# Optimization experiments

Hardware: AMD Instinct MI355X
Metric: run time of the kernel (lower is better)

## Reference

```python
import jax, jax.numpy as jnp
import numpy as np

B, CIN, C, H, T = 8, 64, 64, 62, 400
S = 32              # StateSpaceLayer state_dim default
MID = max(1, C // 16)  # ChannelAttention reduction=16


def _dwconv(x, w, pad):
    # x [B,C,H,W], w [C,1,kh,kw], depthwise conv
    return jax.lax.conv_general_dilated(
        x, w, (1, 1), pad,
        dimension_numbers=('NCHW', 'OIHW', 'NCHW'),
        feature_group_count=x.shape[1])


def _pw(x, w):  # 1x1 conv, w [O,C]
    return jnp.einsum('bchw,oc->bohw', x, w)


def _bn(x, g, b):  # eval-mode BatchNorm with running mean=0, var=1 folded into affine
    return x * g[None, :, None, None] + b[None, :, None, None]


def _chan_attn(x, w1, w2):
    # AdaptiveAvg/MaxPool(1) -> shared MLP -> sigmoid gate
    avg = x.mean(axis=(2, 3))
    mx = x.max(axis=(2, 3))
    fc = lambda v: jax.nn.relu(v @ w1.T) @ w2.T  # Linear weights are [out,in]
    a = jax.nn.sigmoid(fc(avg) + fc(mx))
    return x * a[:, :, None, None]


def _spat_attn(x, w):
    avg = x.mean(axis=1, keepdims=True)
    mx = x.max(axis=1, keepdims=True)
    comb = jnp.concatenate([avg, mx], axis=1)  # [B,2,H,W]
    a = jax.nn.sigmoid(jax.lax.conv_general_dilated(
        comb, w, (1, 1), ((3, 3), (3, 3)),
        dimension_numbers=('NCHW', 'OIHW', 'NCHW')))
    return x * a


def _ssm(x, A, Bv, Cm, D, ln_g, ln_b):
    # Faithful to torch: raw reshape [B,C,H,T] -> [B*H, C, T] (row-major, same as torch)
    b, c, h, t = x.shape
    xs = x.reshape(b * h, c, t)
    seq = jnp.moveaxis(xs, 2, 0)  # [T, N, C]

    def step(state, inp):
        state = state @ A.T + Bv               # state = state A^T + B
        out = jax.nn.gelu(state @ Cm + inp * D, approximate=False)
        return state, out

    init = jnp.zeros((b * h, A.shape[0]), x.dtype)
    _, outs = jax.lax.scan(step, init, seq)    # outs [T, N, C]
    out = jnp.moveaxis(outs, 0, 2).reshape(b, c, h, t)
    out = x + out  # residual (dropout p=0)
    # LayerNorm over channel dim
    y = jnp.moveaxis(out, 1, -1)  # [B,H,T,C]
    mu = y.mean(-1, keepdims=True)
    var = ((y - mu) ** 2).mean(-1, keepdims=True)
    y = (y - mu) / jnp.sqrt(var + 1e-5) * ln_g + ln_b
    return jnp.moveaxis(y, -1, 1)


def _half(x, dwdw, dwpw, dwg, dwb, caw1, caw2, saw,
          d1dw, d1pw, d1g, d1b, A, Bv, Cm, D, lng, lnb):
    pad5 = ((2, 2), (2, 2))
    b1 = jax.nn.relu(_bn(_pw(_dwconv(x, dwdw[0], pad5), dwpw[0]), dwg[0], dwb[0]))
    b2 = jax.nn.relu(_bn(_pw(_dwconv(x, dwdw[1], pad5), dwpw[1]), dwg[1], dwb[1]))
    cb = b1 * _chan_attn(b1, caw1, caw2)       # note: x * ChannelAttention(x) as in source
    cb = _bn(_pw(_dwconv(cb, d1dw, ((0, 0), (1, 1))), d1pw), d1g, d1b)
    cb = jax.nn.sigmoid(cb)
    sb = jax.nn.sigmoid(b2 * _spat_attn(b2, saw))
    return _ssm(cb, A, Bv, Cm, D, lng, lnb) * sb


def setup_inputs() -> dict:
    key = jax.random.key(0)
    ks = jax.random.split(key, 16)
    n = lambda k, shp, s=0.1: jax.random.normal(k, shp, dtype=jnp.float32) * s
    return {
        'x': jax.random.normal(ks[0], (B, CIN, H, T), dtype=jnp.float32),
        'in_w': n(ks[1], (C, CIN)),
        'dw2d_dw': n(ks[2], (2, 2, C, 1, 5, 5)),
        'dw2d_pw': n(ks[3], (2, 2, C, C)),
        'dw2d_g': jnp.ones((2, 2, C), jnp.float32),
        'dw2d_b': jnp.zeros((2, 2, C), jnp.float32),
        'ca_w1': n(ks[4], (2, MID, C)),
        'ca_w2': n(ks[5], (2, C, MID)),
        'sa_w': n(ks[6], (2, 1, 2, 7, 7)),
        'dw1d_dw': n(ks[7], (2, C, 1, 1, 3)),
        'dw1d_pw': n(ks[8], (2, C, C)),
        'dw1d_g': jnp.ones((2, C), jnp.float32),
        'dw1d_b': jnp.zeros((2, C), jnp.float32),
        'ssm_A': n(ks[9], (2, S, S)),
        'ssm_B': n(ks[10], (2, S)),
        'ssm_C': n(ks[11], (2, S, C)),
        'ssm_D': n(ks[12], (2, C)),
        'ln_g': jnp.ones((2, C), jnp.float32),
        'ln_b': jnp.zeros((2, C), jnp.float32),
        'out_w': n(ks[13], (C, C)),
        'out_g': jnp.ones((C,), jnp.float32),
        'out_b': jnp.zeros((C,), jnp.float32),
    }


def reference(x, in_w, dw2d_dw, dw2d_pw, dw2d_g, dw2d_b, ca_w1, ca_w2, sa_w,
              dw1d_dw, dw1d_pw, dw1d_g, dw1d_b, ssm_A, ssm_B, ssm_C, ssm_D,
              ln_g, ln_b, out_w, out_g, out_b):
    h = _pw(x, in_w)
    o = _half(h, dw2d_dw[0], dw2d_pw[0], dw2d_g[0], dw2d_b[0], ca_w1[0], ca_w2[0],
              sa_w[0], dw1d_dw[0], dw1d_pw[0], dw1d_g[0], dw1d_b[0],
              ssm_A[0], ssm_B[0], ssm_C[0], ssm_D[0], ln_g[0], ln_b[0])
    o = o[..., ::-1]  # flip time axis
    o = _half(o, dw2d_dw[1], dw2d_pw[1], dw2d_g[1], dw2d_b[1], ca_w1[1], ca_w2[1],
              sa_w[1], dw1d_dw[1], dw1d_pw[1], dw1d_g[1], dw1d_b[1],
              ssm_A[1], ssm_B[1], ssm_C[1], ssm_D[1], ln_g[1], ln_b[1])
    o = o[..., ::-1]
    return jax.nn.relu(_bn(_pw(o, out_w), out_g, out_b))
```

## Files before the change

kernel.cpp:

```cpp
#include <hip/hip_runtime.h>
#include <math.h>

#define DI __device__ __forceinline__

constexpr int B_ = 8, C_ = 64, H_ = 62, T_ = 400, S_ = 32;
constexpr int HT   = H_ * T_;
constexpr int CHT  = C_ * HT;
constexpr int NPOS = B_ * HT;
constexpr int NTOT = B_ * CHT;

typedef __attribute__((ext_vector_type(8))) short short8;
typedef __attribute__((ext_vector_type(4))) float float4v;

DI float sigmoidf_(float x) { return 1.f / (1.f + expf(-x)); }
DI float gelu_(float x) { return 0.5f * x * (1.f + erff(x * 0.70710678118654752f)); }

template<int ACT> DI float act_(float v) {
  if (ACT == 1) return fmaxf(v, 0.f);
  if (ACT == 2) return sigmoidf_(v);
  return v;
}

DI unsigned short f2b(float f) {
  unsigned int u = __float_as_uint(f);
  u += 0x7FFFu + ((u >> 16) & 1u);
  return (unsigned short)(u >> 16);
}
DI unsigned int pk2(float a, float b) {
  return (unsigned int)f2b(a) | ((unsigned int)f2b(b) << 16);
}

__global__ __launch_bounds__(256) void prep(const float* __restrict__ in_w,
    const float* __restrict__ dwpw, const float* __restrict__ dwg,
    const float* __restrict__ d1pw, const float* __restrict__ d1g,
    const float* __restrict__ outw, const float* __restrict__ outg,
    unsigned short* __restrict__ wf) {
  int idx = blockIdx.x * 256 + threadIdx.x;
  int lane = idx & 63, kc = (idx >> 6) & 1, w = (idx >> 7) & 3, slot = idx >> 9;
  const float* src; const float* g;
  switch (slot) {
    case 0: src = in_w;            g = nullptr;      break;
    case 1: src = dwpw + 0 * 4096; g = dwg + 0 * 64; break;
    case 2: src = dwpw + 1 * 4096; g = dwg + 1 * 64; break;
    case 3: src = d1pw + 0 * 4096; g = d1g + 0 * 64; break;
    case 4: src = dwpw + 2 * 4096; g = dwg + 2 * 64; break;
    case 5: src = dwpw + 3 * 4096; g = dwg + 3 * 64; break;
    case 6: src = d1pw + 1 * 4096; g = d1g + 1 * 64; break;
    default: src = outw;           g = outg;         break;
  }
  int o = w * 16 + (lane & 15);
  float gv = g ? g[o] : 1.f;
  unsigned int pack[4];
  #pragma unroll
  for (int h = 0; h < 4; ++h) {
    int c = kc * 32 + (lane >> 4) * 8 + h * 2;
    pack[h] = pk2(src[o * 64 + c] * gv, src[o * 64 + c + 1] * gv);
  }
  *(uint4*)&wf[idx * 8] = make_uint4(pack[0], pack[1], pack[2], pack[3]);
}

template<int ACT, bool REV, bool SPAT, bool DW13>
__global__ __launch_bounds__(256) void pwk(const float* __restrict__ in,
    const unsigned short* __restrict__ wf, const float* __restrict__ bb,
    const float* __restrict__ ac, const float* __restrict__ w3,
    float* __restrict__ out, float* __restrict__ comb) {
  __shared__ unsigned short Xb[64 * 72];
  const int tid = threadIdx.x;
  const int lane = tid & 63;
  const int wv = tid >> 6;
  const int p0 = blockIdx.x * 64;
  {
    const int ps = (tid & 15) * 4;
    const int cs = (tid >> 4) * 4;
    const int p4 = p0 + ps;
    const int b = p4 / HT, ht = p4 - b * HT;
    const int row = ht / T_, t0 = ht - row * T_;
    const float* rp0 = in + b * CHT + row * T_;
    float xv[4][4];
    #pragma unroll
    for (int cj = 0; cj < 4; ++cj) {
      const int c = cs + cj;
      const float* rp = rp0 + c * HT;
      if constexpr (DW13) {
        float4 xc = *(const float4*)&rp[t0];
        float xm = (t0 > 0)       ? rp[t0 - 1] : 0.f;
        float xp = (t0 < T_ - 4)  ? rp[t0 + 4] : 0.f;
        float s0 = xm * xm, s1 = xc.x * xc.x, s2 = xc.y * xc.y;
        float s3 = xc.z * xc.z, s4 = xc.w * xc.w, s5 = xp * xp;
        float acv = ac[b * 64 + c];
        float c0 = w3[c * 3 + 0] * acv, c1 = w3[c * 3 + 1] * acv,
              c2 = w3[c * 3 + 2] * acv;
        xv[cj][0] = c0 * s0 + c1 * s1 + c2 * s2;
        xv[cj][1] = c0 * s1 + c1 * s2 + c2 * s3;
        xv[cj][2] = c0 * s2 + c1 * s3 + c2 * s4;
        xv[cj][3] = c0 * s3 + c1 * s4 + c2 * s5;
      } else if constexpr (REV) {
        float4 u = *(const float4*)&rp[T_ - 4 - t0];
        xv[cj][0] = u.w; xv[cj][1] = u.z; xv[cj][2] = u.y; xv[cj][3] = u.x;
      } else {
        float4 u = *(const float4*)&rp[t0];
        xv[cj][0] = u.x; xv[cj][1] = u.y; xv[cj][2] = u.z; xv[cj][3] = u.w;
      }
    }
    #pragma unroll
    for (int pi = 0; pi < 4; ++pi) {
      int r = ps + pi;
      int col = cs ^ (((r >> 2) & 7) << 3);
      *(uint2*)&Xb[r * 72 + col] =
          make_uint2(pk2(xv[0][pi], xv[1][pi]), pk2(xv[2][pi], xv[3][pi]));
    }
  }
  short8 af0 = *(const short8*)(wf + ((wv * 2 + 0) * 64 + lane) * 8);
  short8 af1 = *(const short8*)(wf + ((wv * 2 + 1) * 64 + lane) * 8);
  const int m4 = (lane >> 4) * 4;
  float binit[4];
  #pragma unroll
  for (int j = 0; j < 4; ++j) binit[j] = bb ? bb[wv * 16 + m4 + j] : 0.f;
  __syncthreads();
  float4v acc[4];
  #pragma unroll
  for (int nt = 0; nt < 4; ++nt) { acc[nt][0] = acc[nt][1] = acc[nt][2] = acc[nt][3] = 0.f; }
  #pragma unroll
  for (int nt = 0; nt < 4; ++nt) {
    int r = nt * 16 + (lane & 15);
    int sw = ((r >> 2) & 7) << 3;
    int cb0 = ((lane >> 4) * 8) ^ sw;
    int cb1 = (32 + (lane >> 4) * 8) ^ sw;
    short8 b0 = *(const short8*)&Xb[r * 72 + cb0];
    short8 b1 = *(const short8*)&Xb[r * 72 + cb1];
    acc[nt] = __builtin_amdgcn_mfma_f32_16x16x32_bf16(af0, b0, acc[nt], 0, 0, 0);
    acc[nt] = __builtin_amdgcn_mfma_f32_16x16x32_bf16(af1, b1, acc[nt], 0, 0, 0);
  }
  float psum[4], pmaxv[4];
  #pragma unroll
  for (int nt = 0; nt < 4; ++nt) {
    int n = nt * 16 + (lane & 15);
    int p = p0 + n;
    int b = p / HT, ht = p - b * HT;
    float* op = out + b * CHT + ht + (wv * 16 + m4) * HT;
    float s = 0.f, m = -3.4e38f;
    #pragma unroll
    for (int j = 0; j < 4; ++j) {
      float r = act_<ACT>(acc[nt][j] + binit[j]);
      op[j * HT] = r;
      if constexpr (SPAT) { s += r; m = fmaxf(m, r); }
    }
    if constexpr (SPAT) {
      s += __shfl_xor(s, 16); s += __shfl_xor(s, 32);
      m = fmaxf(m, __shfl_xor(m, 16)); m = fmaxf(m, __shfl_xor(m, 32));
      psum[nt] = s; pmaxv[nt] = m;
    }
  }
  if constexpr (SPAT) {
    __shared__ float redS[4][64], redM[4][64];
    if (lane < 16) {
      #pragma unroll
      for (int nt = 0; nt < 4; ++nt) {
        redS[wv][nt * 16 + lane] = psum[nt];
        redM[wv][nt * 16 + lane] = pmaxv[nt];
      }
    }
    __syncthreads();
    if (tid < 64) {
      float s = redS[0][tid] + redS[1][tid] + redS[2][tid] + redS[3][tid];
      float m = fmaxf(fmaxf(redM[0][tid], redM[1][tid]),
                      fmaxf(redM[2][tid], redM[3][tid]));
      int pp = p0 + tid;
      int b2 = pp / HT, ht2 = pp - b2 * HT;
      comb[b2 * 2 * HT + ht2] = s * (1.f / 64.f);
      comb[b2 * 2 * HT + HT + ht2] = m;
    }
  }
}

__global__ __launch_bounds__(256) void dw5dual(const float* __restrict__ in,
    const float* __restrict__ w0_, const float* __restrict__ w1_,
    float* __restrict__ out0, float* __restrict__ out1) {
  const int bc = blockIdx.y;
  const int c = bc & 63;
  int task = blockIdx.x * 256 + threadIdx.x;
  if (task >= 6200) return;
  int h = task / 100;
  int t0 = (task - h * 100) << 2;
  const float* base = in + bc * HT;
  float win[5][12];
  const bool fast = (t0 >= 4) && (t0 <= 392);
  #pragma unroll
  for (int u = 0; u < 5; ++u) {
    int hh = h + u - 2;
    if (hh >= 0 && hh < H_) {
      const float* row = base + hh * T_;
      if (fast) {
        #pragma unroll
        for (int j = 0; j < 3; ++j)
          *(float4*)&win[u][4 * j] = *(const float4*)&row[t0 - 4 + 4 * j];
      } else {
        #pragma unroll
        for (int k = 0; k < 12; ++k) {
          int tt = t0 - 4 + k;
          win[u][k] = (tt >= 0 && tt < T_) ? row[tt] : 0.f;
        }
      }
    } else {
      #pragma unroll
      for (int k = 0; k < 12; ++k) win[u][k] = 0.f;
    }
  }
  float o0[4] = {0.f, 0.f, 0.f, 0.f};
  float o1[4] = {0.f, 0.f, 0.f, 0.f};
  #pragma unroll
  for (int u = 0; u < 5; ++u)
    #pragma unroll
    for (int v = 0; v < 5; ++v) {
      float wa = w0_[c * 25 + u * 5 + v];
      float wb = w1_[c * 25 + u * 5 + v];
      #pragma unroll
      for (int j = 0; j < 4; ++j) {
        float x = win[u][j + v + 2];
        o0[j] += wa * x;
        o1[j] += wb * x;
      }
    }
  *(float4*)&out0[bc * HT + h * T_ + t0] = make_float4(o0[0], o0[1], o0[2], o0[3]);
  *(float4*)&out1[bc * HT + h * T_ + t0] = make_float4(o1[0], o1[1], o1[2], o1[3]);
}

__global__ __launch_bounds__(256) void chanred(const float* __restrict__ in,
    float* __restrict__ sum_, float* __restrict__ max_) {
  int bc = blockIdx.x >> 1, hf = blockIdx.x & 1;
  const float* base = in + (size_t)bc * HT + hf * (HT / 2);
  float s = 0.f, m = -3.4e38f;
  for (int i = threadIdx.x; i < HT / 2; i += 256) {
    float v = base[i];
    s += v; m = fmaxf(m, v);
  }
  #pragma unroll
  for (int off = 32; off > 0; off >>= 1) {
    s += __shfl_down(s, off);
    m = fmaxf(m, __shfl_down(m, off));
  }
  __shared__ float ss[4], sm[4];
  int wv = threadIdx.x >> 6;
  if ((threadIdx.x & 63) == 0) { ss[wv] = s; sm[wv] = m; }
  __syncthreads();
  if (threadIdx.x == 0) {
    float S = ss[0] + ss[1] + ss[2] + ss[3];
    float M = fmaxf(fmaxf(sm[0], sm[1]), fmaxf(sm[2], sm[3]));
    sum_[hf * 512 + bc] = S;
    max_[hf * 512 + bc] = M;
  }
}

__global__ __launch_bounds__(512) void cafc(const float* __restrict__ cs,
    const float* __restrict__ cm, const float* __restrict__ w1,
    const float* __restrict__ w2, float* __restrict__ ac) {
  __shared__ float sa[512], sx[512], hsum[8][4];
  int tid = threadIdx.x;
  sa[tid] = (cs[tid] + cs[512 + tid]) * (1.f / HT);
  sx[tid] = fmaxf(cm[tid], cm[512 + tid]);
  __syncthreads();
  if (tid < 32) {
    int b = tid >> 2, m = tid & 3;
    float s1 = 0.f, s2 = 0.f;
    #pragma unroll
    for (int cc = 0; cc < 64; ++cc) {
      float wv = w1[m * 64 + cc];
      s1 += sa[b * 64 + cc] * wv;
      s2 += sx[b * 64 + cc] * wv;
    }
    hsum[b][m] = fmaxf(s1, 0.f) + fmaxf(s2, 0.f);
  }
  __syncthreads();
  int b = tid >> 6, cc = tid & 63;
  float f = 0.f;
  #pragma unroll
  for (int m = 0; m < 4; ++m) f += hsum[b][m] * w2[cc * 4 + m];
  ac[tid] = sigmoidf_(f);
}

__global__ __launch_bounds__(256) void conv7(const float* __restrict__ comb,
    const float* __restrict__ w, float* __restrict__ as_) {
  __shared__ float sm[2][8][408];
  __shared__ float sw[98];
  const int b = blockIdx.x / 31, hp = blockIdx.x % 31;
  const int h0 = hp * 2;
  const float* cb0 = comb + b * 2 * HT;
  const int tid = threadIdx.x;
  if (tid < 98) sw[tid] = w[tid];
  for (int e = tid; e < 2 * 8 * 408; e += 256) {
    int ci = e / 3264, rem = e - ci * 3264;
    int r = rem / 408, tt = rem - r * 408;
    int hh = h0 - 3 + r, t = tt - 4;
    float v = 0.f;
    if (hh >= 0 && hh < H_ && t >= 0 && t < T_) v = cb0[ci * HT + hh * T_ + t];
    sm[ci][r][tt] = v;
  }
  __syncthreads();
  for (int o = tid; o < 800; o += 256) {
    int oh = o / 400, ot = o - oh * 400;
    float acc = 0.f;
    #pragma unroll
    for (int ci = 0; ci < 2; ++ci)
      #pragma unroll
      for (int u = 0; u < 7; ++u)
        #pragma unroll
        for (int v = 0; v < 7; ++v)
          acc += sw[ci * 49 + u * 7 + v] * sm[ci][oh + u][ot + v + 1];
    as_[b * HT + (h0 + oh) * T_ + ot] = sigmoidf_(acc);
  }
}

__global__ __launch_bounds__(1024) void ssmctA(const float* __restrict__ A_,
    const float* __restrict__ Bv_, float* __restrict__ Pg, float* __restrict__ qg) {
  const int hf = blockIdx.x;
  const float* A = A_ + hf * 1024;
  const float* Bv = Bv_ + hf * 32;
  __shared__ float Pbuf[2][32 * 33];
  __shared__ float qbuf[2][32];
  const int tid = threadIdx.x;
  float* Pc = Pbuf[0]; float* Pn = Pbuf[1];
  float* qc = qbuf[0]; float* qn = qbuf[1];
  Pc[(tid >> 5) * 33 + (tid & 31)] = A[tid];
  if (tid < 32) qc[tid] = Bv[tid];
  __syncthreads();
  for (int i = 0; i < 9; ++i) {
    Pg[(hf * 9 + i) * 1024 + tid] = Pc[(tid >> 5) * 33 + (tid & 31)];
    if (tid < 32) qg[(hf * 9 + i) * 32 + tid] = qc[tid];
    if (i == 8) break;
    const int r = tid >> 5, cc = tid & 31;
    float s0 = 0.f, s1 = 0.f, s2 = 0.f, s3 = 0.f;
    #pragma unroll
    for (int k = 0; k < 32; k += 4) {
      s0 += Pc[r * 33 + k + 0] * Pc[(k + 0) * 33 + cc];
      s1 += Pc[r * 33 + k + 1] * Pc[(k + 1) * 33 + cc];
      s2 += Pc[r * 33 + k + 2] * Pc[(k + 2) * 33 + cc];
      s3 += Pc[r * 33 + k + 3] * Pc[(k + 3) * 33 + cc];
    }
    float qv = 0.f;
    if (tid < 32) {
      float a0 = 0.f, a1 = 0.f;
      #pragma unroll
      for (int k = 0; k < 32; k += 2) {
        a0 += Pc[tid * 33 + k] * qc[k];
        a1 += Pc[tid * 33 + k + 1] * qc[k + 1];
      }
      qv = qc[tid] + a0 + a1;
    }
    Pn[r * 33 + cc] = s0 + s1 + s2 + s3;
    if (tid < 32) qn[tid] = qv;
    __syncthreads();
    float* tp = Pc; Pc = Pn; Pn = tp;
    float* tq = qc; qc = qn; qn = tq;
  }
}

__global__ __launch_bounds__(1024) void ssmctB(const float* __restrict__ Pg,
    const float* __restrict__ qg, const float* __restrict__ Cm_,
    float* __restrict__ ct) {
  const int hf = blockIdx.y;
  __shared__ float P[9][32][33];
  __shared__ float q[9][32];
  __shared__ float Cs[32 * 64];
  __shared__ float st[32][33];
  const int tid = threadIdx.x;
  #pragma unroll
  for (int i = 0; i < 9; ++i) {
    int rem = tid;
    P[i][rem >> 5][rem & 31] = Pg[(hf * 9 + i) * 1024 + rem];
  }
  if (tid < 9 * 32) q[tid >> 5][tid & 31] = qg[hf * 9 * 32 + tid];
  for (int e = tid; e < 2048; e += 1024) Cs[e] = Cm_[hf * 2048 + e];
  __syncthreads();
  const int grp = tid >> 5, j = tid & 31;
  const int tIdx = blockIdx.x * 32 + grp;
  const int n = tIdx + 1;
  float s = 0.f;
  #pragma unroll
  for (int i = 0; i < 9; ++i) {
    st[grp][j] = s;
    float a0 = q[i][j], a1 = 0.f;
    #pragma unroll
    for (int k = 0; k < 32; k += 2) {
      a0 += P[i][j][k] * st[grp][k];
      a1 += P[i][j][k + 1] * st[grp][k + 1];
    }
    s = ((n >> i) & 1) ? (a0 + a1) : s;
  }
  st[grp][j] = s;
  __syncthreads();
  #pragma unroll
  for (int e0 = 0; e0 < 2048; e0 += 1024) {
    int e = e0 + tid;
    int ts = e >> 6, c = e & 63;
    float a0 = 0.f, a1 = 0.f;
    #pragma unroll
    for (int k = 0; k < 32; k += 2) {
      a0 += st[ts][k] * Cs[k * 64 + c];
      a1 += st[ts][k + 1] * Cs[(k + 1) * 64 + c];
    }
    int tg = blockIdx.x * 32 + ts;
    if (tg < T_) ct[(hf * T_ + tg) * 64 + c] = a0 + a1;
  }
}

__global__ __launch_bounds__(256) void k8(const float* __restrict__ cb,
    const float* __restrict__ b2, const float* __restrict__ as_,
    const float* __restrict__ ct, const float* __restrict__ D,
    const float* __restrict__ lng, const float* __restrict__ lnb,
    float* __restrict__ out, int rev) {
  __shared__ float ct_s[64 * 65];
  __shared__ float red[4 * 2 * 66];
  const int tid = threadIdx.x;
  const int pl = tid & 63, wg = tid >> 6;
  const int p0 = blockIdx.x * 64;
  #pragma unroll
  for (int k = 0; k < 16; ++k) {
    int idx = k * 256 + tid;
    int r = idx >> 6, c2 = idx & 63;
    int t = (p0 + r) % T_;
    ct_s[r * 65 + c2] = ct[t * C_ + c2];
  }
  const int p = p0 + pl;
  const int b = p / HT, ht = p - b * HT;
  const int h = ht / T_, t = ht - h * T_;
  __syncthreads();
  const float* cbp = cb + b * CHT + ht;
  const float* b2p = b2 + b * CHT + ht;
  float o[16];
  float sum = 0.f;
  #pragma unroll
  for (int i = 0; i < 16; ++i) {
    int c = wg * 16 + i;
    float xv = cbp[c * HT];
    int c2 = (62 * c + h) & 63;
    float u = ct_s[pl * 65 + c2] + xv * D[c2];
    float v = xv + gelu_(u);
    o[i] = v; sum += v;
  }
  red[wg * 132 + pl] = sum;
  __syncthreads();
  float S = red[0 * 132 + pl] + red[1 * 132 + pl] + red[2 * 132 + pl] + red[3 * 132 + pl];
  float mu = S * (1.f / 64.f);
  float vp = 0.f;
  #pragma unroll
  for (int i = 0; i < 16; ++i) { float d = o[i] - mu; vp += d * d; }
  red[wg * 132 + 66 + pl] = vp;
  __syncthreads();
  float Q = red[0 * 132 + 66 + pl] + red[1 * 132 + 66 + pl] +
            red[2 * 132 + 66 + pl] + red[3 * 132 + 66 + pl];
  float rstd = rsqrtf(Q * (1.f / 64.f) + 1e-5f);
  float av = as_[p];
  int htw = rev ? (h * T_ + (T_ - 1 - t)) : ht;
  float* op = out + b * CHT + htw;
  #pragma unroll
  for (int i = 0; i < 16; ++i) {
    int c = wg * 16 + i;
    float y = (o[i] - mu) * rstd * lng[c] + lnb[c];
    float bv = b2p[c * HT];
    op[c * HT] = y * sigmoidf_(bv * bv * av);
  }
}

extern "C" void kernel_launch(void* const* d_in, const int* in_sizes, int n_in,
                              void* d_out, int out_size, void* d_ws, size_t ws_size,
                              hipStream_t stream) {
  const float* x    = (const float*)d_in[0];
  const float* in_w = (const float*)d_in[1];
  const float* dwdw = (const float*)d_in[2];
  const float* dwpw = (const float*)d_in[3];
  const float* dwg  = (const float*)d_in[4];
  const float* dwb  = (const float*)d_in[5];
  const float* caw1 = (const float*)d_in[6];
  const float* caw2 = (const float*)d_in[7];
  const float* saw  = (const float*)d_in[8];
  const float* d1dw = (const float*)d_in[9];
  const float* d1pw = (const float*)d_in[10];
  const float* d1g  = (const float*)d_in[11];
  const float* d1b  = (const float*)d_in[12];
  const float* ssmA = (const float*)d_in[13];
  const float* ssmBv= (const float*)d_in[14];
  const float* ssmC = (const float*)d_in[15];
  const float* ssmD = (const float*)d_in[16];
  const float* lng  = (const float*)d_in[17];
  const float* lnb  = (const float*)d_in[18];
  const float* outw = (const float*)d_in[19];
  const float* outg = (const float*)d_in[20];
  const float* outb = (const float*)d_in[21];

  size_t need = (size_t)(3 * (size_t)NTOT + 2 * NPOS + NPOS + 1024 + 1024 + 512
                         + 2 * T_ * C_ + 2 * 9 * 1024 + 2 * 9 * 32 + 16384) * 4;
  if (ws_size < need) return;

  float* W0 = (float*)d_ws;
  float* W1 = W0 + NTOT;
  float* W2 = W1 + NTOT;
  float* comb  = W2 + NTOT;
  float* as_   = comb + 2 * NPOS;
  float* casum = as_ + NPOS;
  float* camax = casum + 1024;
  float* ac    = camax + 1024;
  float* ct    = ac + 512;
  float* Pg    = ct + 2 * T_ * C_;
  float* qg    = Pg + 2 * 9 * 1024;
  unsigned short* Wbf = (unsigned short*)(qg + 2 * 9 * 32);

  prep<<<16, 256, 0, stream>>>(in_w, dwpw, dwg, d1pw, d1g, outw, outg, Wbf);
  ssmctA<<<2, 1024, 0, stream>>>(ssmA, ssmBv, Pg, qg);
  ssmctB<<<dim3(13, 2), 1024, 0, stream>>>(Pg, qg, ssmC, ct);
  pwk<0, false, false, false><<<3100, 256, 0, stream>>>(x, Wbf + 0 * 4096, nullptr,
                                                        nullptr, nullptr, W0, nullptr);

  auto run_half = [&](int hf, float* X, float* Fa, float* Fb) {
    const float* dw0 = dwdw + (hf * 2 + 0) * C_ * 25;
    const float* dw1 = dwdw + (hf * 2 + 1) * C_ * 25;
    const float* b0  = dwb + (hf * 2 + 0) * C_;
    const float* b1w = dwb + (hf * 2 + 1) * C_;
    dw5dual<<<dim3(25, 512), 256, 0, stream>>>(X, dw0, dw1, Fa, Fb);
    pwk<1, false, false, false><<<3100, 256, 0, stream>>>(Fa, Wbf + (1 + hf * 3) * 4096,
                                                          b0, nullptr, nullptr, X, nullptr);
    pwk<1, false, true, false><<<3100, 256, 0, stream>>>(Fb, Wbf + (2 + hf * 3) * 4096,
                                                         b1w, nullptr, nullptr, Fa, comb);
    chanred<<<1024, 256, 0, stream>>>(X, casum, camax);
    cafc<<<1, 512, 0, stream>>>(casum, camax, caw1 + hf * 4 * 64, caw2 + hf * 64 * 4, ac);
    conv7<<<248, 256, 0, stream>>>(comb, saw + hf * 98, as_);
    pwk<2, false, false, true><<<3100, 256, 0, stream>>>(X, Wbf + (3 + hf * 3) * 4096,
                                                         d1b + hf * C_, ac,
                                                         d1dw + hf * C_ * 3, Fb, nullptr);
    k8<<<3100, 256, 0, stream>>>(Fb, Fa, as_, ct + hf * T_ * C_,
                                 ssmD + hf * C_, lng + hf * C_, lnb + hf * C_,
                                 X, hf == 0 ? 1 : 0);
  };

  run_half(0, W0, W1, W2);
  run_half(1, W0, W1, W2);
  pwk<1, true, false, false><<<3100, 256, 0, stream>>>(W0, Wbf + 7 * 4096, outb,
                                                       nullptr, nullptr,
                                                       (float*)d_out, nullptr);
}
```

Before: 421.4 us.

## Store all intermediate activation buffers in bf16 instead of fp32

Switches the three large workspace buffers (W0/W1/W2) from fp32 to bf16 across every producer and consumer kernel: the pointwise MFMA kernels, the depthwise 5x5 conv, the channel reduction and the SSM/LayerNorm kernel. Since the pipeline is memory-bound over roughly 50M-element tensors, this halves the global read and write traffic of every stage. The cost is extra rounding of intermediates, which lowers accuracy and could push results past tolerance.

```diff
diff --git a/kernel.cpp b/kernel.cpp
--- a/kernel.cpp
+++ b/kernel.cpp
@@ -11,6 +11,7 @@
 
 typedef __attribute__((ext_vector_type(8))) short short8;
 typedef __attribute__((ext_vector_type(4))) float float4v;
+typedef unsigned short bh;
 
 DI float sigmoidf_(float x) { return 1.f / (1.f + expf(-x)); }
 DI float gelu_(float x) { return 0.5f * x * (1.f + erff(x * 0.70710678118654752f)); }
@@ -21,11 +22,12 @@
   return v;
 }
 
-DI unsigned short f2b(float f) {
+DI bh f2b(float f) {
   unsigned int u = __float_as_uint(f);
   u += 0x7FFFu + ((u >> 16) & 1u);
-  return (unsigned short)(u >> 16);
-}
+  return (bh)(u >> 16);
+}
+DI float b2f(bh u) { return __uint_as_float(((unsigned int)u) << 16); }
 DI unsigned int pk2(float a, float b) {
   return (unsigned int)f2b(a) | ((unsigned int)f2b(b) << 16);
 }
@@ -34,7 +36,7 @@
     const float* __restrict__ dwpw, const float* __restrict__ dwg,
     const float* __restrict__ d1pw, const float* __restrict__ d1g,
     const float* __restrict__ outw, const float* __restrict__ outg,
-    unsigned short* __restrict__ wf) {
+    bh* __restrict__ wf) {
   int idx = blockIdx.x * 256 + threadIdx.x;
   int lane = idx & 63, kc = (idx >> 6) & 1, w = (idx >> 7) & 3, slot = idx >> 9;
   const float* src; const float* g;
@@ -59,12 +61,12 @@
   *(uint4*)&wf[idx * 8] = make_uint4(pack[0], pack[1], pack[2], pack[3]);
 }
 
-template<int ACT, bool REV, bool SPAT, bool DW13>
-__global__ __launch_bounds__(256) void pwk(const float* __restrict__ in,
-    const unsigned short* __restrict__ wf, const float* __restrict__ bb,
+template<int ACT, bool REV, bool SPAT, bool DW13, bool INF32, bool OUTF32>
+__global__ __launch_bounds__(256) void pwk(const void* __restrict__ in_,
+    const bh* __restrict__ wf, const float* __restrict__ bb,
     const float* __restrict__ ac, const float* __restrict__ w3,
-    float* __restrict__ out, float* __restrict__ comb) {
-  __shared__ unsigned short Xb[64 * 72];
+    void* __restrict__ out_, float* __restrict__ comb) {
+  __shared__ bh Xb[64 * 72];
   const int tid = threadIdx.x;
   const int lane = tid & 63;
   const int wv = tid >> 6;
@@ -75,18 +77,39 @@
     const int p4 = p0 + ps;
     const int b = p4 / HT, ht = p4 - b * HT;
     const int row = ht / T_, t0 = ht - row * T_;
-    const float* rp0 = in + b * CHT + row * T_;
-    float xv[4][4];
-    #pragma unroll
-    for (int cj = 0; cj < 4; ++cj) {
-      const int c = cs + cj;
-      const float* rp = rp0 + c * HT;
-      if constexpr (DW13) {
-        float4 xc = *(const float4*)&rp[t0];
-        float xm = (t0 > 0)       ? rp[t0 - 1] : 0.f;
-        float xp = (t0 < T_ - 4)  ? rp[t0 + 4] : 0.f;
-        float s0 = xm * xm, s1 = xc.x * xc.x, s2 = xc.y * xc.y;
-        float s3 = xc.z * xc.z, s4 = xc.w * xc.w, s5 = xp * xp;
+    unsigned int packed[4][2];
+    if constexpr (INF32) {
+      const float* rp0 = (const float*)in_ + b * CHT + row * T_;
+      float xv[4][4];
+      #pragma unroll
+      for (int cj = 0; cj < 4; ++cj) {
+        const float* rp = rp0 + (cs + cj) * HT;
+        if constexpr (REV) {
+          float4 u = *(const float4*)&rp[T_ - 4 - t0];
+          xv[cj][0] = u.w; xv[cj][1] = u.z; xv[cj][2] = u.y; xv[cj][3] = u.x;
+        } else {
+          float4 u = *(const float4*)&rp[t0];
+          xv[cj][0] = u.x; xv[cj][1] = u.y; xv[cj][2] = u.z; xv[cj][3] = u.w;
+        }
+      }
+      #pragma unroll
+      for (int pi = 0; pi < 4; ++pi) {
+        packed[pi][0] = pk2(xv[0][pi], xv[1][pi]);
+        packed[pi][1] = pk2(xv[2][pi], xv[3][pi]);
+      }
+    } else if constexpr (DW13) {
+      const bh* rp0 = (const bh*)in_ + b * CHT + row * T_;
+      float xv[4][4];
+      #pragma unroll
+      for (int cj = 0; cj < 4; ++cj) {
+        const int c = cs + cj;
+        const bh* rp = rp0 + c * HT;
+        ushort4 u = *(const ushort4*)&rp[t0];
+        float x0 = b2f(u.x), x1 = b2f(u.y), x2 = b2f(u.z), x3 = b2f(u.w);
+        float xm = (t0 > 0)      ? b2f(rp[t0 - 1]) : 0.f;
+        float xp = (t0 < T_ - 4) ? b2f(rp[t0 + 4]) : 0.f;
+        float s0 = xm * xm, s1 = x0 * x0, s2 = x1 * x1;
+        float s3 = x2 * x2, s4 = x3 * x3, s5 = xp * xp;
         float acv = ac[b * 64 + c];
         float c0 = w3[c * 3 + 0] * acv, c1 = w3[c * 3 + 1] * acv,
               c2 = w3[c * 3 + 2] * acv;
@@ -94,20 +117,38 @@
         xv[cj][1] = c0 * s1 + c1 * s2 + c2 * s3;
         xv[cj][2] = c0 * s2 + c1 * s3 + c2 * s4;
         xv[cj][3] = c0 * s3 + c1 * s4 + c2 * s5;
-      } else if constexpr (REV) {
-        float4 u = *(const float4*)&rp[T_ - 4 - t0];
-        xv[cj][0] = u.w; xv[cj][1] = u.z; xv[cj][2] = u.y; xv[cj][3] = u.x;
-      } else {
-        float4 u = *(const float4*)&rp[t0];
-        xv[cj][0] = u.x; xv[cj][1] = u.y; xv[cj][2] = u.z; xv[cj][3] = u.w;
+      }
+      #pragma unroll
+      for (int pi = 0; pi < 4; ++pi) {
+        packed[pi][0] = pk2(xv[0][pi], xv[1][pi]);
+        packed[pi][1] = pk2(xv[2][pi], xv[3][pi]);
+      }
+    } else {
+      const bh* rp0 = (const bh*)in_ + b * CHT + row * T_;
+      bh us[4][4];
+      #pragma unroll
+      for (int cj = 0; cj < 4; ++cj) {
+        const bh* rp = rp0 + (cs + cj) * HT;
+        ushort4 u;
+        if constexpr (REV) {
+          u = *(const ushort4*)&rp[T_ - 4 - t0];
+          us[cj][0] = u.w; us[cj][1] = u.z; us[cj][2] = u.y; us[cj][3] = u.x;
+        } else {
+          u = *(const ushort4*)&rp[t0];
+          us[cj][0] = u.x; us[cj][1] = u.y; us[cj][2] = u.z; us[cj][3] = u.w;
+        }
+      }
+      #pragma unroll
+      for (int pi = 0; pi < 4; ++pi) {
+        packed[pi][0] = (unsigned int)us[0][pi] | ((unsigned int)us[1][pi] << 16);
+        packed[pi][1] = (unsigned int)us[2][pi] | ((unsigned int)us[3][pi] << 16);
       }
     }
     #pragma unroll
     for (int pi = 0; pi < 4; ++pi) {
       int r = ps + pi;
       int col = cs ^ (((r >> 2) & 7) << 3);
-      *(uint2*)&Xb[r * 72 + col] =
-          make_uint2(pk2(xv[0][pi], xv[1][pi]), pk2(xv[2][pi], xv[3][pi]));
+      *(uint2*)&Xb[r * 72 + col] = make_uint2(packed[pi][0], packed[pi][1]);
     }
   }
   short8 af0 = *(const short8*)(wf + ((wv * 2 + 0) * 64 + lane) * 8);
@@ -137,13 +178,23 @@
     int n = nt * 16 + (lane & 15);
     int p = p0 + n;
     int b = p / HT, ht = p - b * HT;
-    float* op = out + b * CHT + ht + (wv * 16 + m4) * HT;
     float s = 0.f, m = -3.4e38f;
-    #pragma unroll
-    for (int j = 0; j < 4; ++j) {
-      float r = act_<ACT>(acc[nt][j] + binit[j]);
-      op[j * HT] = r;
-      if constexpr (SPAT) { s += r; m = fmaxf(m, r); }
+    if constexpr (OUTF32) {
+      float* op = (float*)out_ + b * CHT + ht + (wv * 16 + m4) * HT;
+      #pragma unroll
+      for (int j = 0; j < 4; ++j) {
+        float r = act_<ACT>(acc[nt][j] + binit[j]);
+        op[j * HT] = r;
+        if constexpr (SPAT) { s += r; m = fmaxf(m, r); }
+      }
+    } else {
+      bh* op = (bh*)out_ + b * CHT + ht + (wv * 16 + m4) * HT;
+      #pragma unroll
+      for (int j = 0; j < 4; ++j) {
+        float r = act_<ACT>(acc[nt][j] + binit[j]);
+        op[j * HT] = f2b(r);
+        if constexpr (SPAT) { s += r; m = fmaxf(m, r); }
+      }
     }
     if constexpr (SPAT) {
       s += __shfl_xor(s, 16); s += __shfl_xor(s, 32);
@@ -173,32 +224,35 @@
   }
 }
 
-__global__ __launch_bounds__(256) void dw5dual(const float* __restrict__ in,
+__global__ __launch_bounds__(256) void dw5dual(const bh* __restrict__ in,
     const float* __restrict__ w0_, const float* __restrict__ w1_,
-    float* __restrict__ out0, float* __restrict__ out1) {
+    bh* __restrict__ out0, bh* __restrict__ out1) {
   const int bc = blockIdx.y;
   const int c = bc & 63;
   int task = blockIdx.x * 256 + threadIdx.x;
   if (task >= 6200) return;
   int h = task / 100;
   int t0 = (task - h * 100) << 2;
-  const float* base = in + bc * HT;
+  const bh* base = in + bc * HT;
   float win[5][12];
   const bool fast = (t0 >= 4) && (t0 <= 392);
   #pragma unroll
   for (int u = 0; u < 5; ++u) {
     int hh = h + u - 2;
     if (hh >= 0 && hh < H_) {
-      const float* row = base + hh * T_;
+      const bh* row = base + hh * T_;
       if (fast) {
         #pragma unroll
-        for (int j = 0; j < 3; ++j)
-          *(float4*)&win[u][4 * j] = *(const float4*)&row[t0 - 4 + 4 * j];
+        for (int j = 0; j < 3; ++j) {
+          ushort4 q = *(const ushort4*)&row[t0 - 4 + 4 * j];
+          win[u][4 * j + 0] = b2f(q.x); win[u][4 * j + 1] = b2f(q.y);
+          win[u][4 * j + 2] = b2f(q.z); win[u][4 * j + 3] = b2f(q.w);
+        }
       } else {
         #pragma unroll
         for (int k = 0; k < 12; ++k) {
           int tt = t0 - 4 + k;
-          win[u][k] = (tt >= 0 && tt < T_) ? row[tt] : 0.f;
+          win[u][k] = (tt >= 0 && tt < T_) ? b2f(row[tt]) : 0.f;
         }
       }
     } else {
@@ -221,18 +275,22 @@
         o1[j] += wb * x;
       }
     }
-  *(float4*)&out0[bc * HT + h * T_ + t0] = make_float4(o0[0], o0[1], o0[2], o0[3]);
-  *(float4*)&out1[bc * HT + h * T_ + t0] = make_float4(o1[0], o1[1], o1[2], o1[3]);
-}
-
-__global__ __launch_bounds__(256) void chanred(const float* __restrict__ in,
+  ushort4 r0, r1;
+  r0.x = f2b(o0[0]); r0.y = f2b(o0[1]); r0.z = f2b(o0[2]); r0.w = f2b(o0[3]);
+  r1.x = f2b(o1[0]); r1.y = f2b(o1[1]); r1.z = f2b(o1[2]); r1.w = f2b(o1[3]);
+  *(ushort4*)&out0[bc * HT + h * T_ + t0] = r0;
+  *(ushort4*)&out1[bc * HT + h * T_ + t0] = r1;
+}
+
+__global__ __launch_bounds__(256) void chanred(const bh* __restrict__ in,
     float* __restrict__ sum_, float* __restrict__ max_) {
   int bc = blockIdx.x >> 1, hf = blockIdx.x & 1;
-  const float* base = in + (size_t)bc * HT + hf * (HT / 2);
+  const bh* base = in + (size_t)bc * HT + hf * (HT / 2);
   float s = 0.f, m = -3.4e38f;
-  for (int i = threadIdx.x; i < HT / 2; i += 256) {
-    float v = base[i];
-    s += v; m = fmaxf(m, v);
+  for (int i = threadIdx.x * 2; i < HT / 2; i += 512) {
+    ushort2 q = *(const ushort2*)&base[i];
+    float v0 = b2f(q.x), v1 = b2f(q.y);
+    s += v0 + v1; m = fmaxf(m, fmaxf(v0, v1));
   }
   #pragma unroll
   for (int off = 32; off > 0; off >>= 1) {
@@ -403,11 +461,11 @@
   }
 }
 
-__global__ __launch_bounds__(256) void k8(const float* __restrict__ cb,
-    const float* __restrict__ b2, const float* __restrict__ as_,
+__global__ __launch_bounds__(256) void k8(const bh* __restrict__ cb,
+    const bh* __restrict__ b2, const float* __restrict__ as_,
     const float* __restrict__ ct, const float* __restrict__ D,
     const float* __restrict__ lng, const float* __restrict__ lnb,
-    float* __restrict__ out, int rev) {
+    bh* __restrict__ out, int rev) {
   __shared__ float ct_s[64 * 65];
   __shared__ float red[4 * 2 * 66];
   const int tid = threadIdx.x;
@@ -424,14 +482,14 @@
   const int b = p / HT, ht = p - b * HT;
   const int h = ht / T_, t = ht - h * T_;
   __syncthreads();
-  const float* cbp = cb + b * CHT + ht;
-  const float* b2p = b2 + b * CHT + ht;
+  const bh* cbp = cb + b * CHT + ht;
+  const bh* b2p = b2 + b * CHT + ht;
   float o[16];
   float sum = 0.f;
   #pragma unroll
   for (int i = 0; i < 16; ++i) {
     int c = wg * 16 + i;
-    float xv = cbp[c * HT];
+    float xv = b2f(cbp[c * HT]);
     int c2 = (62 * c + h) & 63;
     float u = ct_s[pl * 65 + c2] + xv * D[c2];
     float v = xv + gelu_(u);
@@ -451,13 +509,13 @@
   float rstd = rsqrtf(Q * (1.f / 64.f) + 1e-5f);
   float av = as_[p];
   int htw = rev ? (h * T_ + (T_ - 1 - t)) : ht;
-  float* op = out + b * CHT + htw;
+  bh* op = out + b * CHT + htw;
   #pragma unroll
   for (int i = 0; i < 16; ++i) {
     int c = wg * 16 + i;
     float y = (o[i] - mu) * rstd * lng[c] + lnb[c];
-    float bv = b2p[c * HT];
-    op[c * HT] = y * sigmoidf_(bv * bv * av);
+    float bv = b2f(b2p[c * HT]);
+    op[c * HT] = f2b(y * sigmoidf_(bv * bv * av));
   }
 }
 
@@ -487,14 +545,17 @@
   const float* outg = (const float*)d_in[20];
   const float* outb = (const float*)d_in[21];
 
-  size_t need = (size_t)(3 * (size_t)NTOT + 2 * NPOS + NPOS + 1024 + 1024 + 512
-                         + 2 * T_ * C_ + 2 * 9 * 1024 + 2 * 9 * 32 + 16384) * 4;
+  size_t bigBytes = (size_t)3 * NTOT * 2;
+  size_t fCount = (size_t)(2 * NPOS + NPOS + 1024 + 1024 + 512
+                           + 2 * T_ * C_ + 2 * 9 * 1024 + 2 * 9 * 32);
+  size_t need = bigBytes + fCount * 4 + (size_t)8 * 4096 * 2;
   if (ws_size < need) return;
 
-  float* W0 = (float*)d_ws;
-  float* W1 = W0 + NTOT;
-  float* W2 = W1 + NTOT;
-  float* comb  = W2 + NTOT;
+  bh* W0 = (bh*)d_ws;
+  bh* W1 = W0 + NTOT;
+  bh* W2 = W1 + NTOT;
+  float* fbase = (float*)((char*)d_ws + bigBytes);
+  float* comb  = fbase;
   float* as_   = comb + 2 * NPOS;
   float* casum = as_ + NPOS;
   float* camax = casum + 1024;
@@ -502,30 +563,30 @@
   float* ct    = ac + 512;
   float* Pg    = ct + 2 * T_ * C_;
   float* qg    = Pg + 2 * 9 * 1024;
-  unsigned short* Wbf = (unsigned short*)(qg + 2 * 9 * 32);
+  bh* Wbf = (bh*)(qg + 2 * 9 * 32);
 
   prep<<<16, 256, 0, stream>>>(in_w, dwpw, dwg, d1pw, d1g, outw, outg, Wbf);
   ssmctA<<<2, 1024, 0, stream>>>(ssmA, ssmBv, Pg, qg);
   ssmctB<<<dim3(13, 2), 1024, 0, stream>>>(Pg, qg, ssmC, ct);
-  pwk<0, false, false, false><<<3100, 256, 0, stream>>>(x, Wbf + 0 * 4096, nullptr,
-                                                        nullptr, nullptr, W0, nullptr);
-
-  auto run_half = [&](int hf, float* X, float* Fa, float* Fb) {
+  pwk<0, false, false, false, true, false><<<3100, 256, 0, stream>>>(
+      x, Wbf + 0 * 4096, nullptr, nullptr, nullptr, W0, nullptr);
+
+  auto run_half = [&](int hf, bh* X, bh* Fa, bh* Fb) {
     const float* dw0 = dwdw + (hf * 2 + 0) * C_ * 25;
     const float* dw1 = dwdw + (hf * 2 + 1) * C_ * 25;
     const float* b0  = dwb + (hf * 2 + 0) * C_;
     const float* b1w = dwb + (hf * 2 + 1) * C_;
     dw5dual<<<dim3(25, 512), 256, 0, stream>>>(X, dw0, dw1, Fa, Fb);
-    pwk<1, false, false, false><<<3100, 256, 0, stream>>>(Fa, Wbf + (1 + hf * 3) * 4096,
-                                                          b0, nullptr, nullptr, X, nullptr);
-    pwk<1, false, true, false><<<3100, 256, 0, stream>>>(Fb, Wbf + (2 + hf * 3) * 4096,
-                                                         b1w, nullptr, nullptr, Fa, comb);
+    pwk<1, false, false, false, false, false><<<3100, 256, 0, stream>>>(
+        Fa, Wbf + (1 + hf * 3) * 4096, b0, nullptr, nullptr, X, nullptr);
+    pwk<1, false, true, false, false, false><<<3100, 256, 0, stream>>>(
+        Fb, Wbf + (2 + hf * 3) * 4096, b1w, nullptr, nullptr, Fa, comb);
     chanred<<<1024, 256, 0, stream>>>(X, casum, camax);
     cafc<<<1, 512, 0, stream>>>(casum, camax, caw1 + hf * 4 * 64, caw2 + hf * 64 * 4, ac);
     conv7<<<248, 256, 0, stream>>>(comb, saw + hf * 98, as_);
-    pwk<2, false, false, true><<<3100, 256, 0, stream>>>(X, Wbf + (3 + hf * 3) * 4096,
-                                                         d1b + hf * C_, ac,
-                                                         d1dw + hf * C_ * 3, Fb, nullptr);
+    pwk<2, false, false, true, false, false><<<3100, 256, 0, stream>>>(
+        X, Wbf + (3 + hf * 3) * 4096, d1b + hf * C_, ac, d1dw + hf * C_ * 3,
+        Fb, nullptr);
     k8<<<3100, 256, 0, stream>>>(Fb, Fa, as_, ct + hf * T_ * C_,
                                  ssmD + hf * C_, lng + hf * C_, lnb + hf * C_,
                                  X, hf == 0 ? 1 : 0);
@@ -533,7 +594,6 @@
 
   run_half(0, W0, W1, W2);
   run_half(1, W0, W1, W2);
-  pwk<1, true, false, false><<<3100, 256, 0, stream>>>(W0, Wbf + 7 * 4096, outb,
-                                                       nullptr, nullptr,
-                                                       (float*)d_out, nullptr);
-}
+  pwk<1, true, false, false, false, true><<<3100, 256, 0, stream>>>(
+      W0, Wbf + 7 * 4096, outb, nullptr, nullptr, (float*)d_out, nullptr);
+}
```

Result: slower. 446.5 us (+6.0%).
